# Kernel tuning notes

Measured on AMD Instinct MI355X. Metric: run time of the kernel, lower is better.

The kernel has to match this reference:

```python
import jax, jax.numpy as jnp
import numpy as np

T = 8192        # tokens (batch*seq)
D = 1024        # d_model
H = 4096        # expert hidden = 4*d_model
E = 16          # num_expert
K = 2           # moe_top_k


def setup_inputs() -> dict:
    key = jax.random.key(0)
    ks = jax.random.split(key, 7)
    s_in = 1.0 / np.sqrt(D)
    s_h = 1.0 / np.sqrt(H)
    return {
        "moe_inp": jax.random.normal(ks[0], (T, D), dtype=jnp.float32),
        "Wg": jax.random.normal(ks[1], (D, E), dtype=jnp.float32) * s_in,
        "bg": jnp.zeros((E,), dtype=jnp.float32),
        "W1": jax.random.normal(ks[2], (E, D, H), dtype=jnp.float32) * s_in,
        "b1": jnp.zeros((E, H), dtype=jnp.float32),
        "W2": jax.random.normal(ks[3], (E, H, D), dtype=jnp.float32) * s_h,
        "b2": jnp.zeros((E, D), dtype=jnp.float32),
    }


def reference(moe_inp, Wg, bg, W1, b1, W2, b2):
    # --- NaiveGate: linear -> top-k -> softmax over selected logits ---
    logits = moe_inp @ Wg + bg                      # [T, E]
    topk_val, topk_idx = jax.lax.top_k(logits, K)   # [T, K]
    gate_score = jax.nn.softmax(topk_val, axis=-1)  # [T, K]

    # Per-(token, expert) combine weight: sum of gate scores of slots routed to e.
    # Equivalent to scatter(dispatch) -> expert MLP -> gather(combine) weighted sum.
    onehot = jax.nn.one_hot(topk_idx, E, dtype=moe_inp.dtype)  # [T, K, E]
    comb_w = jnp.einsum('tk,tke->te', gate_score, onehot)      # [T, E]

    out = jnp.zeros_like(moe_inp)
    for e in range(E):  # fixed small expert count
        h = jax.nn.relu(moe_inp @ W1[e] + b1[e])   # [T, H]
        y = h @ W2[e] + b2[e]                      # [T, D]
        out = out + comb_w[:, e:e + 1] * y
    return out
```

## Files before the change

kernel.cpp:

```cpp
#include <hip/hip_runtime.h>
#include <hip/hip_bf16.h>
#include <stdint.h>


#define Tn 8192
#define Dn 1024
#define Hn 4096
#define En 16

typedef __attribute__((ext_vector_type(8))) short bf16x8;
typedef __attribute__((ext_vector_type(4))) float f32x4;

__device__ __forceinline__ unsigned short f2bf(float f) {
    union { __hip_bfloat16 h; unsigned short u; } cv;
    cv.h = __float2bfloat16(f);
    return cv.u;
}

__device__ __forceinline__ void gload_lds16(const void* gptr, void* lptr) {
    __builtin_amdgcn_global_load_lds(
        (const __attribute__((address_space(1))) uint32_t*)gptr,
        (__attribute__((address_space(3))) uint32_t*)lptr, 16, 0, 0);
}

__device__ __forceinline__ int find_e(const int* __restrict__ mb, int gm) {
    int e = 0;
#pragma unroll
    for (int i = 1; i < En; i++) e += (mb[i] <= gm) ? 1 : 0;
    return e;
}

__device__ __forceinline__ void waitvm8() { asm volatile("s_waitcnt vmcnt(8)" ::: "memory"); }
__device__ __forceinline__ void waitvm4() { asm volatile("s_waitcnt vmcnt(4)" ::: "memory"); }
__device__ __forceinline__ void waitvm0() { asm volatile("s_waitcnt vmcnt(0)" ::: "memory"); }
__device__ __forceinline__ void waitlgkm0() { asm volatile("s_waitcnt lgkmcnt(0)" ::: "memory"); }
__device__ __forceinline__ void barrier_raw() { asm volatile("s_barrier" ::: "memory"); }

__device__ __forceinline__ bool better(float va, int ia, float vb, int ib) {
    return (va > vb) || (va == vb && ia < ib);
}

__global__ __launch_bounds__(256) void gate_kernel(
    const float* __restrict__ x, const float* __restrict__ Wg,
    const float* __restrict__ bg,
    int* cnt, int* tok_e, int* tok_pos, float* tok_w)
{
    __shared__ float wgt[16 * 1028];
    int tid = threadIdx.x;
    int t0 = blockIdx.x * 16;

#pragma unroll
    for (int i = 0; i < 64; i++) {
        int idx = i * 256 + tid;
        int k = idx >> 4, e = idx & 15;
        wgt[e * 1028 + k] = Wg[idx];
    }
    __syncthreads();

    int tok = tid >> 4, e = tid & 15;
    const float4* xr = reinterpret_cast<const float4*>(x + (size_t)(t0 + tok) * Dn);
    const float4* wr = reinterpret_cast<const float4*>(&wgt[e * 1028]);
    float acc = 0.f;
#pragma unroll 8
    for (int q = 0; q < 256; q++) {
        float4 xv = xr[q], wv = wr[q];
        acc += xv.x * wv.x + xv.y * wv.y + xv.z * wv.z + xv.w * wv.w;
    }
    acc += bg[e];

    float v0 = acc, v1 = -1e30f;
    int i0 = e, i1 = -1;
#pragma unroll
    for (int m = 1; m < 16; m <<= 1) {
        float ov0 = __shfl_xor(v0, m, 16); int oi0 = __shfl_xor(i0, m, 16);
        float ov1 = __shfl_xor(v1, m, 16); int oi1 = __shfl_xor(i1, m, 16);
        if (better(ov0, oi0, v0, i0)) {
            if (better(v0, i0, ov1, oi1)) { v1 = v0; i1 = i0; }
            else                          { v1 = ov1; i1 = oi1; }
            v0 = ov0; i0 = oi0;
        } else if (better(ov0, oi0, v1, i1)) {
            v1 = ov0; i1 = oi0;
        }
    }
    if (e == 0) {
        float ex = __expf(v1 - v0);
        float w0 = 1.f / (1.f + ex);
        float w1 = ex / (1.f + ex);
        int p0 = atomicAdd(&cnt[i0], 1);
        int p1 = atomicAdd(&cnt[i1], 1);
        int t = t0 + tok;
        tok_e[t * 2 + 0] = i0; tok_e[t * 2 + 1] = i1;
        tok_pos[t * 2 + 0] = p0; tok_pos[t * 2 + 1] = p1;
        tok_w[t * 2 + 0] = w0; tok_w[t * 2 + 1] = w1;
    }
}

__global__ void scan_kernel(const int* cnt, int* base, int* mb)
{
    if (threadIdx.x == 0 && blockIdx.x == 0) {
        int b = 0, m = 0;
        for (int e = 0; e < En; e++) {
            base[e] = b; mb[e] = m;
            b += cnt[e];
            m += (cnt[e] + 255) >> 8;
        }
        base[En] = b; mb[En] = m;
    }
}

__global__ __launch_bounds__(256) void gather_kernel(
    const float* __restrict__ x, const int* tok_e, const int* tok_pos,
    const int* base, unsigned short* xg)
{
    int t = blockIdx.x; int tid = threadIdx.x;
    int e0 = tok_e[2 * t], e1 = tok_e[2 * t + 1];
    int r0 = base[e0] + tok_pos[2 * t];
    int r1 = base[e1] + tok_pos[2 * t + 1];
    float4 v = *reinterpret_cast<const float4*>(x + (size_t)t * Dn + tid * 4);
    ushort4 u;
    u.x = f2bf(v.x); u.y = f2bf(v.y); u.z = f2bf(v.z); u.w = f2bf(v.w);
    *reinterpret_cast<ushort4*>(xg + (size_t)r0 * Dn + tid * 4) = u;
    *reinterpret_cast<ushort4*>(xg + (size_t)r1 * Dn + tid * 4) = u;
}

__global__ __launch_bounds__(512) void convT_kernel(
    const float* __restrict__ src, unsigned short* __restrict__ dst, int R, int C)
{
    int e = blockIdx.z;
    const float* s = src + (size_t)e * R * C;
    unsigned short* d = dst + (size_t)e * R * C;
    __shared__ float tile[64][65];
    int r0 = blockIdx.y * 64, c0 = blockIdx.x * 64;
    int tr = threadIdx.x >> 4;
    int tc4 = (threadIdx.x & 15) * 4;
    float4 v0 = *reinterpret_cast<const float4*>(s + (size_t)(r0 + tr) * C + c0 + tc4);
    float4 v1 = *reinterpret_cast<const float4*>(s + (size_t)(r0 + tr + 32) * C + c0 + tc4);
    tile[tr][tc4 + 0] = v0.x; tile[tr][tc4 + 1] = v0.y;
    tile[tr][tc4 + 2] = v0.z; tile[tr][tc4 + 3] = v0.w;
    tile[tr + 32][tc4 + 0] = v1.x; tile[tr + 32][tc4 + 1] = v1.y;
    tile[tr + 32][tc4 + 2] = v1.z; tile[tr + 32][tc4 + 3] = v1.w;
    __syncthreads();
    ushort4 u0, u1;
    u0.x = f2bf(tile[tc4 + 0][tr]);      u1.x = f2bf(tile[tc4 + 0][tr + 32]);
    u0.y = f2bf(tile[tc4 + 1][tr]);      u1.y = f2bf(tile[tc4 + 1][tr + 32]);
    u0.z = f2bf(tile[tc4 + 2][tr]);      u1.z = f2bf(tile[tc4 + 2][tr + 32]);
    u0.w = f2bf(tile[tc4 + 3][tr]);      u1.w = f2bf(tile[tc4 + 3][tr + 32]);
    *reinterpret_cast<ushort4*>(d + (size_t)(c0 + tr) * R + r0 + tc4) = u0;
    *reinterpret_cast<ushort4*>(d + (size_t)(c0 + tr + 32) * R + r0 + tc4) = u1;
}

template<bool G1>
__global__ __launch_bounds__(512, 2) void gemm8p_kernel(
    const unsigned short* __restrict__ Ag, const unsigned short* __restrict__ Bg,
    const float* __restrict__ bias, unsigned short* __restrict__ outb,
    float* __restrict__ outf, size_t ystride,
    const int* __restrict__ cnt, const int* __restrict__ base,
    const int* __restrict__ mb)
{
    constexpr int KDIM = G1 ? Dn : Hn;
    constexpr int KLEN = G1 ? Dn : (Hn / 2);
    constexpr int NOUT = G1 ? Hn : Dn;
    constexpr int NT = KLEN / 32;
    __shared__ unsigned short ldsA[4][256 * 32];
    __shared__ unsigned short ldsB[4][256 * 32];

    int bid = blockIdx.x;
    int xcd = bid & 7;
    int slot = bid >> 3;
    int totalgm = mb[En];
    int rounds = G1 ? ((totalgm + 15) >> 4) : ((totalgm + 31) >> 5);

    int tid = threadIdx.x;
    int lane = tid & 63;
    int wid = tid >> 6;
    int wr = wid >> 2, wc = wid & 3;
    int lr16 = lane & 15, lk = lane >> 4;
    int lj = (lane >> 4) * 4;

    int ja0 = tid;        int ra0 = ja0 >> 2; int ca0 = (ja0 & 3) ^ ((ra0 >> 1) & 3);
    int ja1 = tid + 512;  int ra1 = ja1 >> 2; int ca1 = (ja1 & 3) ^ ((ra1 >> 1) & 3);

    int aoff[8], boff[4];
#pragma unroll
    for (int m = 0; m < 8; m++) {
        int row = wr * 128 + m * 16 + lr16;
        aoff[m] = row * 32 + ((lk ^ ((row >> 1) & 3)) << 3);
    }
#pragma unroll
    for (int n = 0; n < 4; n++) {
        int row = wc * 64 + n * 16 + lr16;
        boff[n] = row * 32 + ((lk ^ ((row >> 1) & 3)) << 3);
    }

    for (int r = 0; r < rounds; r++) {
        int gm, ntile, kh;
        if constexpr (G1) {
            gm = r * 16 + (slot >> 1);
            ntile = xcd * 2 + (slot & 1);
            kh = 0;
        } else {
            gm = r * 32 + slot;
            ntile = xcd >> 1;
            kh = xcd & 1;
        }
        if (gm >= totalgm) continue;

        int e = find_e(mb, gm);
        int mtile = gm - mb[e];
        int M_e = cnt[e];
        int m0 = mtile * 256, n0 = ntile * 256;
        int kbase = kh * KLEN;
        int rowbase0 = base[e] + m0;
        const unsigned short* Ab = Ag + (size_t)rowbase0 * KDIM + kbase;
        const unsigned short* Bb = Bg + (size_t)e * NOUT * KDIM + (size_t)n0 * KDIM + kbase;

        const unsigned short* aSrc0 = Ab + (size_t)ra0 * KDIM + ca0 * 8;
        const unsigned short* aSrc1 = Ab + (size_t)ra1 * KDIM + ca1 * 8;
        const unsigned short* bSrc0 = Bb + (size_t)ra0 * KDIM + ca0 * 8;
        const unsigned short* bSrc1 = Bb + (size_t)ra1 * KDIM + ca1 * 8;

        f32x4 acc[8][4];
#pragma unroll
        for (int m = 0; m < 8; m++)
#pragma unroll
            for (int n = 0; n < 4; n++) acc[m][n] = (f32x4){0.f, 0.f, 0.f, 0.f};

        auto stageA = [&](int t) {
            char* sa = (char*)ldsA[t & 3];
            int k0 = t * 32;
            gload_lds16(aSrc0 + k0, sa + ja0 * 16);
            gload_lds16(aSrc1 + k0, sa + ja1 * 16);
        };
        auto stageB = [&](int t) {
            char* sb = (char*)ldsB[t & 3];
            int k0 = t * 32;
            gload_lds16(bSrc0 + k0, sb + ja0 * 16);
            gload_lds16(bSrc1 + k0, sb + ja1 * 16);
        };

        stageB(0); stageA(0);
        stageB(1); stageA(1);
        stageB(2); stageA(2);
        waitvm8();
        barrier_raw();

#pragma unroll 4
        for (int t = 0; t < NT; ++t) {
            const unsigned short* sa = ldsA[t & 3];
            const unsigned short* sb = ldsB[t & 3];
            bf16x8 a[4], b[4];
#pragma unroll
            for (int m = 0; m < 4; m++) a[m] = *(const bf16x8*)(sa + aoff[m]);
#pragma unroll
            for (int n = 0; n < 4; n++) b[n] = *(const bf16x8*)(sb + boff[n]);
            if (t + 3 < NT) stageB(t + 3);
            barrier_raw();
            waitlgkm0();
            __builtin_amdgcn_s_setprio(1);
#pragma unroll
            for (int m = 0; m < 4; m++)
#pragma unroll
                for (int n = 0; n < 4; n++)
                    acc[m][n] = __builtin_amdgcn_mfma_f32_16x16x32_bf16(b[n], a[m], acc[m][n], 0, 0, 0);
            __builtin_amdgcn_s_setprio(0);
            barrier_raw();
#pragma unroll
            for (int m = 0; m < 4; m++) a[m] = *(const bf16x8*)(sa + aoff[m + 4]);
            if (t + 3 < NT) stageA(t + 3);
            barrier_raw();
            waitlgkm0();
            __builtin_amdgcn_s_setprio(1);
#pragma unroll
            for (int m = 0; m < 4; m++)
#pragma unroll
                for (int n = 0; n < 4; n++)
                    acc[m + 4][n] = __builtin_amdgcn_mfma_f32_16x16x32_bf16(b[n], a[m], acc[m + 4][n], 0, 0, 0);
            __builtin_amdgcn_s_setprio(0);
            if (t < NT - 3)       waitvm8();
            else if (t == NT - 3) waitvm4();
            else if (t == NT - 2) waitvm0();
            barrier_raw();
        }

        bool addb = G1 || (kh == 0);
        const float* be = bias + (size_t)e * NOUT;
        float* yb = outf + (G1 ? 0 : (size_t)kh * ystride);
#pragma unroll
        for (int m = 0; m < 8; m++) {
            int rt = wr * 128 + m * 16 + lr16;
            if (m0 + rt < M_e) {
                size_t rowoff = (size_t)(rowbase0 + rt) * NOUT;
#pragma unroll
                for (int n = 0; n < 4; n++) {
                    int col0 = n0 + wc * 64 + n * 16 + lj;
                    float4 bs = addb ? *reinterpret_cast<const float4*>(be + col0)
                                     : (float4){0.f, 0.f, 0.f, 0.f};
                    float v0 = acc[m][n][0] + bs.x;
                    float v1 = acc[m][n][1] + bs.y;
                    float v2 = acc[m][n][2] + bs.z;
                    float v3 = acc[m][n][3] + bs.w;
                    if constexpr (G1) {
                        ushort4 u;
                        u.x = f2bf(fmaxf(v0, 0.f));
                        u.y = f2bf(fmaxf(v1, 0.f));
                        u.z = f2bf(fmaxf(v2, 0.f));
                        u.w = f2bf(fmaxf(v3, 0.f));
                        *reinterpret_cast<ushort4*>(outb + rowoff + col0) = u;
                    } else {
                        float4 o = {v0, v1, v2, v3};
                        *reinterpret_cast<float4*>(yb + rowoff + col0) = o;
                    }
                }
            }
        }
    }
}

__global__ __launch_bounds__(256) void combine_kernel(
    const float* __restrict__ y, size_t ystride,
    const int* __restrict__ tok_e, const int* __restrict__ tok_pos,
    const int* __restrict__ base, const float* __restrict__ tok_w,
    float* __restrict__ out)
{
    int t = blockIdx.x, tid = threadIdx.x;
    int e0 = tok_e[2 * t], e1 = tok_e[2 * t + 1];
    int r0 = base[e0] + tok_pos[2 * t];
    int r1 = base[e1] + tok_pos[2 * t + 1];
    float w0 = tok_w[2 * t], w1 = tok_w[2 * t + 1];
    const float* y1 = y + ystride;
    float4 a0 = *reinterpret_cast<const float4*>(y  + (size_t)r0 * Dn + tid * 4);
    float4 a1 = *reinterpret_cast<const float4*>(y1 + (size_t)r0 * Dn + tid * 4);
    float4 b0 = *reinterpret_cast<const float4*>(y  + (size_t)r1 * Dn + tid * 4);
    float4 b1 = *reinterpret_cast<const float4*>(y1 + (size_t)r1 * Dn + tid * 4);
    float4 o;
    o.x = w0 * (a0.x + a1.x) + w1 * (b0.x + b1.x);
    o.y = w0 * (a0.y + a1.y) + w1 * (b0.y + b1.y);
    o.z = w0 * (a0.z + a1.z) + w1 * (b0.z + b1.z);
    o.w = w0 * (a0.w + a1.w) + w1 * (b0.w + b1.w);
    *reinterpret_cast<float4*>(out + (size_t)t * Dn + tid * 4) = o;
}

extern "C" void kernel_launch(void* const* d_in, const int* in_sizes, int n_in,
                              void* d_out, int out_size, void* d_ws, size_t ws_size,
                              hipStream_t stream)
{
    const float* x  = (const float*)d_in[0];
    const float* Wg = (const float*)d_in[1];
    const float* bg = (const float*)d_in[2];
    const float* W1 = (const float*)d_in[3];
    const float* b1 = (const float*)d_in[4];
    const float* W2 = (const float*)d_in[5];
    const float* b2 = (const float*)d_in[6];
    float* out = (float*)d_out;

    char* ws = (char*)d_ws;
    size_t off = 0;
    auto alloc = [&](size_t bytes) {
        size_t o = off; off += (bytes + 255) & ~(size_t)255; return o;
    };
    const int ROWS = Tn * 2;
    const int RCAP = ROWS + 256;
    const size_t YSTR = (size_t)RCAP * Dn;

    unsigned short* Wt = (unsigned short*)(ws + alloc((size_t)En * Hn * Dn * 2));
    unsigned short* xg = (unsigned short*)(ws + alloc((size_t)RCAP * Dn * 2));
    unsigned short* hg = (unsigned short*)(ws + alloc((size_t)RCAP * Hn * 2));
    float* yv      = (float*)(ws + alloc(2 * YSTR * 4));
    int*   cnt     = (int*)(ws + alloc(En * 4));
    int*   base    = (int*)(ws + alloc((En + 1) * 4));
    int*   mb      = (int*)(ws + alloc((En + 1) * 4));
    int*   tok_e   = (int*)(ws + alloc(Tn * 2 * 4));
    int*   tok_pos = (int*)(ws + alloc(Tn * 2 * 4));
    float* tok_w   = (float*)(ws + alloc(Tn * 2 * 4));
    (void)ws_size; (void)in_sizes; (void)n_in; (void)out_size;

    hipMemsetAsync(cnt, 0, En * 4, stream);

    gate_kernel<<<Tn / 16, 256, 0, stream>>>(x, Wg, bg, cnt, tok_e, tok_pos, tok_w);
    scan_kernel<<<1, 64, 0, stream>>>(cnt, base, mb);
    gather_kernel<<<Tn, 256, 0, stream>>>(x, tok_e, tok_pos, base, xg);

    convT_kernel<<<dim3(Hn / 64, Dn / 64, En), 512, 0, stream>>>(W1, Wt, Dn, Hn);
    gemm8p_kernel<true><<<256, 512, 0, stream>>>(
        xg, Wt, b1, hg, nullptr, 0, cnt, base, mb);

    convT_kernel<<<dim3(Dn / 64, Hn / 64, En), 512, 0, stream>>>(W2, Wt, Hn, Dn);
    gemm8p_kernel<false><<<256, 512, 0, stream>>>(
        hg, Wt, b2, nullptr, yv, YSTR, cnt, base, mb);

    combine_kernel<<<Tn, 256, 0, stream>>>(yv, YSTR, tok_e, tok_pos, base, tok_w, out);
}
```

Baseline: 737.2 us.

## Switch grouped GEMM to BK=64 double-buffered pipeline and bf16 partial outputs

Restructures the expert GEMM main loop from a 4-stage BK=32 pipeline with split A/B staging and several barriers per step into a 2-stage BK=64 double buffer. It uses one vmcnt(0) wait and one barrier per K step, with an 8-way XOR swizzle on LDS rows. The second GEMM now writes its split-K partial results as bf16 instead of fp32, and the combine kernel reads them back as bf16. This halves the partial-output write and read traffic, at the cost of extra rounding in the partial sums. The shallower pipeline also risks exposing more global-load latency.

After: 753.1 us. 2.2% more time.

```diff
diff --git a/kernel.cpp b/kernel.cpp
--- a/kernel.cpp
+++ b/kernel.cpp
@@ -16,6 +16,11 @@
     cv.h = __float2bfloat16(f);
     return cv.u;
 }
+__device__ __forceinline__ float bf2f(unsigned short u) {
+    union { unsigned int i; float f; } cv;
+    cv.i = ((unsigned int)u) << 16;
+    return cv.f;
+}
 
 __device__ __forceinline__ void gload_lds16(const void* gptr, void* lptr) {
     __builtin_amdgcn_global_load_lds(
@@ -30,10 +35,7 @@
     return e;
 }
 
-__device__ __forceinline__ void waitvm8() { asm volatile("s_waitcnt vmcnt(8)" ::: "memory"); }
-__device__ __forceinline__ void waitvm4() { asm volatile("s_waitcnt vmcnt(4)" ::: "memory"); }
-__device__ __forceinline__ void waitvm0() { asm volatile("s_waitcnt vmcnt(0)" ::: "memory"); }
-__device__ __forceinline__ void waitlgkm0() { asm volatile("s_waitcnt lgkmcnt(0)" ::: "memory"); }
+__device__ __forceinline__ void waitvm0()  { asm volatile("s_waitcnt vmcnt(0)" ::: "memory"); }
 __device__ __forceinline__ void barrier_raw() { asm volatile("s_barrier" ::: "memory"); }
 
 __device__ __forceinline__ bool better(float va, int ia, float vb, int ib) {
@@ -150,19 +152,19 @@
 }
 
 template<bool G1>
-__global__ __launch_bounds__(512, 2) void gemm8p_kernel(
+__global__ __launch_bounds__(512, 2) void gemmk_kernel(
     const unsigned short* __restrict__ Ag, const unsigned short* __restrict__ Bg,
     const float* __restrict__ bias, unsigned short* __restrict__ outb,
-    float* __restrict__ outf, size_t ystride,
+    size_t ystride,
     const int* __restrict__ cnt, const int* __restrict__ base,
     const int* __restrict__ mb)
 {
     constexpr int KDIM = G1 ? Dn : Hn;
     constexpr int KLEN = G1 ? Dn : (Hn / 2);
     constexpr int NOUT = G1 ? Hn : Dn;
-    constexpr int NT = KLEN / 32;
-    __shared__ unsigned short ldsA[4][256 * 32];
-    __shared__ unsigned short ldsB[4][256 * 32];
+    constexpr int NT = KLEN / 64;
+    __shared__ unsigned short ldsA[2][256 * 64];
+    __shared__ unsigned short ldsB[2][256 * 64];
 
     int bid = blockIdx.x;
     int xcd = bid & 7;
@@ -175,21 +177,25 @@
     int wid = tid >> 6;
     int wr = wid >> 2, wc = wid & 3;
     int lr16 = lane & 15, lk = lane >> 4;
-    int lj = (lane >> 4) * 4;
-
-    int ja0 = tid;        int ra0 = ja0 >> 2; int ca0 = (ja0 & 3) ^ ((ra0 >> 1) & 3);
-    int ja1 = tid + 512;  int ra1 = ja1 >> 2; int ca1 = (ja1 & 3) ^ ((ra1 >> 1) & 3);
-
-    int aoff[8], boff[4];
+    int lj = lk * 4;
+
+    int r0t = tid >> 3;
+    int col8 = (tid & 7) ^ (r0t & 7);
+
+    int aoff[8][2], boff[4][2];
 #pragma unroll
     for (int m = 0; m < 8; m++) {
         int row = wr * 128 + m * 16 + lr16;
-        aoff[m] = row * 32 + ((lk ^ ((row >> 1) & 3)) << 3);
+#pragma unroll
+        for (int kk = 0; kk < 2; kk++)
+            aoff[m][kk] = row * 64 + (((kk * 4 + lk) ^ (row & 7)) << 3);
     }
 #pragma unroll
     for (int n = 0; n < 4; n++) {
         int row = wc * 64 + n * 16 + lr16;
-        boff[n] = row * 32 + ((lk ^ ((row >> 1) & 3)) << 3);
+#pragma unroll
+        for (int kk = 0; kk < 2; kk++)
+            boff[n][kk] = row * 64 + (((kk * 4 + lk) ^ (row & 7)) << 3);
     }
 
     for (int r = 0; r < rounds; r++) {
@@ -214,10 +220,8 @@
         const unsigned short* Ab = Ag + (size_t)rowbase0 * KDIM + kbase;
         const unsigned short* Bb = Bg + (size_t)e * NOUT * KDIM + (size_t)n0 * KDIM + kbase;
 
-        const unsigned short* aSrc0 = Ab + (size_t)ra0 * KDIM + ca0 * 8;
-        const unsigned short* aSrc1 = Ab + (size_t)ra1 * KDIM + ca1 * 8;
-        const unsigned short* bSrc0 = Bb + (size_t)ra0 * KDIM + ca0 * 8;
-        const unsigned short* bSrc1 = Bb + (size_t)ra1 * KDIM + ca1 * 8;
+        const unsigned short* aSrc = Ab + (size_t)r0t * KDIM + col8 * 8;
+        const unsigned short* bSrc = Bb + (size_t)r0t * KDIM + col8 * 8;
 
         f32x4 acc[8][4];
 #pragma unroll
@@ -225,66 +229,55 @@
 #pragma unroll
             for (int n = 0; n < 4; n++) acc[m][n] = (f32x4){0.f, 0.f, 0.f, 0.f};
 
-        auto stageA = [&](int t) {
-            char* sa = (char*)ldsA[t & 3];
-            int k0 = t * 32;
-            gload_lds16(aSrc0 + k0, sa + ja0 * 16);
-            gload_lds16(aSrc1 + k0, sa + ja1 * 16);
+        auto stage = [&](int t) {
+            char* sa = (char*)ldsA[t & 1];
+            char* sb = (char*)ldsB[t & 1];
+            int k0 = t * 64;
+#pragma unroll
+            for (int i = 0; i < 4; i++) {
+                gload_lds16(aSrc + (size_t)(i * 64) * KDIM + k0, sa + (tid + i * 512) * 16);
+                gload_lds16(bSrc + (size_t)(i * 64) * KDIM + k0, sb + (tid + i * 512) * 16);
+            }
         };
-        auto stageB = [&](int t) {
-            char* sb = (char*)ldsB[t & 3];
-            int k0 = t * 32;
-            gload_lds16(bSrc0 + k0, sb + ja0 * 16);
-            gload_lds16(bSrc1 + k0, sb + ja1 * 16);
-        };
-
-        stageB(0); stageA(0);
-        stageB(1); stageA(1);
-        stageB(2); stageA(2);
-        waitvm8();
-        barrier_raw();
-
-#pragma unroll 4
+
+        stage(0);
+
         for (int t = 0; t < NT; ++t) {
-            const unsigned short* sa = ldsA[t & 3];
-            const unsigned short* sb = ldsB[t & 3];
-            bf16x8 a[4], b[4];
-#pragma unroll
-            for (int m = 0; m < 4; m++) a[m] = *(const bf16x8*)(sa + aoff[m]);
-#pragma unroll
-            for (int n = 0; n < 4; n++) b[n] = *(const bf16x8*)(sb + boff[n]);
-            if (t + 3 < NT) stageB(t + 3);
+            waitvm0();
             barrier_raw();
-            waitlgkm0();
-            __builtin_amdgcn_s_setprio(1);
-#pragma unroll
-            for (int m = 0; m < 4; m++)
-#pragma unroll
-                for (int n = 0; n < 4; n++)
-                    acc[m][n] = __builtin_amdgcn_mfma_f32_16x16x32_bf16(b[n], a[m], acc[m][n], 0, 0, 0);
-            __builtin_amdgcn_s_setprio(0);
-            barrier_raw();
-#pragma unroll
-            for (int m = 0; m < 4; m++) a[m] = *(const bf16x8*)(sa + aoff[m + 4]);
-            if (t + 3 < NT) stageA(t + 3);
-            barrier_raw();
-            waitlgkm0();
-            __builtin_amdgcn_s_setprio(1);
-#pragma unroll
-            for (int m = 0; m < 4; m++)
-#pragma unroll
-                for (int n = 0; n < 4; n++)
-                    acc[m + 4][n] = __builtin_amdgcn_mfma_f32_16x16x32_bf16(b[n], a[m], acc[m + 4][n], 0, 0, 0);
-            __builtin_amdgcn_s_setprio(0);
-            if (t < NT - 3)       waitvm8();
-            else if (t == NT - 3) waitvm4();
-            else if (t == NT - 2) waitvm0();
-            barrier_raw();
+            if (t + 1 < NT) stage(t + 1);
+            asm volatile("" ::: "memory");
+            const unsigned short* sa = ldsA[t & 1];
+            const unsigned short* sb = ldsB[t & 1];
+#pragma unroll
+            for (int kk = 0; kk < 2; kk++) {
+                bf16x8 a[4], b[4];
+#pragma unroll
+                for (int n = 0; n < 4; n++) b[n] = *(const bf16x8*)(sb + boff[n][kk]);
+#pragma unroll
+                for (int m = 0; m < 4; m++) a[m] = *(const bf16x8*)(sa + aoff[m][kk]);
+                __builtin_amdgcn_s_setprio(1);
+#pragma unroll
+                for (int m = 0; m < 4; m++)
+#pragma unroll
+                    for (int n = 0; n < 4; n++)
+                        acc[m][n] = __builtin_amdgcn_mfma_f32_16x16x32_bf16(b[n], a[m], acc[m][n], 0, 0, 0);
+                __builtin_amdgcn_s_setprio(0);
+#pragma unroll
+                for (int m = 0; m < 4; m++) a[m] = *(const bf16x8*)(sa + aoff[m + 4][kk]);
+                __builtin_amdgcn_s_setprio(1);
+#pragma unroll
+                for (int m = 0; m < 4; m++)
+#pragma unroll
+                    for (int n = 0; n < 4; n++)
+                        acc[m + 4][n] = __builtin_amdgcn_mfma_f32_16x16x32_bf16(b[n], a[m], acc[m + 4][n], 0, 0, 0);
+                __builtin_amdgcn_s_setprio(0);
+            }
         }
 
         bool addb = G1 || (kh == 0);
         const float* be = bias + (size_t)e * NOUT;
-        float* yb = outf + (G1 ? 0 : (size_t)kh * ystride);
+        unsigned short* ob = outb + (G1 ? 0 : (size_t)kh * ystride);
 #pragma unroll
         for (int m = 0; m < 8; m++) {
             int rt = wr * 128 + m * 16 + lr16;
@@ -299,17 +292,17 @@
                     float v1 = acc[m][n][1] + bs.y;
                     float v2 = acc[m][n][2] + bs.z;
                     float v3 = acc[m][n][3] + bs.w;
+                    ushort4 u;
                     if constexpr (G1) {
-                        ushort4 u;
                         u.x = f2bf(fmaxf(v0, 0.f));
                         u.y = f2bf(fmaxf(v1, 0.f));
                         u.z = f2bf(fmaxf(v2, 0.f));
                         u.w = f2bf(fmaxf(v3, 0.f));
-                        *reinterpret_cast<ushort4*>(outb + rowoff + col0) = u;
                     } else {
-                        float4 o = {v0, v1, v2, v3};
-                        *reinterpret_cast<float4*>(yb + rowoff + col0) = o;
+                        u.x = f2bf(v0); u.y = f2bf(v1);
+                        u.z = f2bf(v2); u.w = f2bf(v3);
                     }
+                    *reinterpret_cast<ushort4*>(ob + rowoff + col0) = u;
                 }
             }
         }
@@ -317,7 +310,7 @@
 }
 
 __global__ __launch_bounds__(256) void combine_kernel(
-    const float* __restrict__ y, size_t ystride,
+    const unsigned short* __restrict__ y, size_t ystride,
     const int* __restrict__ tok_e, const int* __restrict__ tok_pos,
     const int* __restrict__ base, const float* __restrict__ tok_w,
     float* __restrict__ out)
@@ -327,16 +320,16 @@
     int r0 = base[e0] + tok_pos[2 * t];
     int r1 = base[e1] + tok_pos[2 * t + 1];
     float w0 = tok_w[2 * t], w1 = tok_w[2 * t + 1];
-    const float* y1 = y + ystride;
-    float4 a0 = *reinterpret_cast<const float4*>(y  + (size_t)r0 * Dn + tid * 4);
-    float4 a1 = *reinterpret_cast<const float4*>(y1 + (size_t)r0 * Dn + tid * 4);
-    float4 b0 = *reinterpret_cast<const float4*>(y  + (size_t)r1 * Dn + tid * 4);
-    float4 b1 = *reinterpret_cast<const float4*>(y1 + (size_t)r1 * Dn + tid * 4);
+    const unsigned short* y1 = y + ystride;
+    ushort4 a0 = *reinterpret_cast<const ushort4*>(y  + (size_t)r0 * Dn + tid * 4);
+    ushort4 a1 = *reinterpret_cast<const ushort4*>(y1 + (size_t)r0 * Dn + tid * 4);
+    ushort4 b0 = *reinterpret_cast<const ushort4*>(y  + (size_t)r1 * Dn + tid * 4);
+    ushort4 b1 = *reinterpret_cast<const ushort4*>(y1 + (size_t)r1 * Dn + tid * 4);
     float4 o;
-    o.x = w0 * (a0.x + a1.x) + w1 * (b0.x + b1.x);
-    o.y = w0 * (a0.y + a1.y) + w1 * (b0.y + b1.y);
-    o.z = w0 * (a0.z + a1.z) + w1 * (b0.z + b1.z);
-    o.w = w0 * (a0.w + a1.w) + w1 * (b0.w + b1.w);
+    o.x = w0 * (bf2f(a0.x) + bf2f(a1.x)) + w1 * (bf2f(b0.x) + bf2f(b1.x));
+    o.y = w0 * (bf2f(a0.y) + bf2f(a1.y)) + w1 * (bf2f(b0.y) + bf2f(b1.y));
+    o.z = w0 * (bf2f(a0.z) + bf2f(a1.z)) + w1 * (bf2f(b0.z) + bf2f(b1.z));
+    o.w = w0 * (bf2f(a0.w) + bf2f(a1.w)) + w1 * (bf2f(b0.w) + bf2f(b1.w));
     *reinterpret_cast<float4*>(out + (size_t)t * Dn + tid * 4) = o;
 }
 
@@ -365,7 +358,7 @@
     unsigned short* Wt = (unsigned short*)(ws + alloc((size_t)En * Hn * Dn * 2));
     unsigned short* xg = (unsigned short*)(ws + alloc((size_t)RCAP * Dn * 2));
     unsigned short* hg = (unsigned short*)(ws + alloc((size_t)RCAP * Hn * 2));
-    float* yv      = (float*)(ws + alloc(2 * YSTR * 4));
+    unsigned short* yv = (unsigned short*)(ws + alloc(2 * YSTR * 2));
     int*   cnt     = (int*)(ws + alloc(En * 4));
     int*   base    = (int*)(ws + alloc((En + 1) * 4));
     int*   mb      = (int*)(ws + alloc((En + 1) * 4));
@@ -381,12 +374,12 @@
     gather_kernel<<<Tn, 256, 0, stream>>>(x, tok_e, tok_pos, base, xg);
 
     convT_kernel<<<dim3(Hn / 64, Dn / 64, En), 512, 0, stream>>>(W1, Wt, Dn, Hn);
-    gemm8p_kernel<true><<<256, 512, 0, stream>>>(
-        xg, Wt, b1, hg, nullptr, 0, cnt, base, mb);
+    gemmk_kernel<true><<<256, 512, 0, stream>>>(
+        xg, Wt, b1, hg, 0, cnt, base, mb);
 
     convT_kernel<<<dim3(Dn / 64, Hn / 64, En), 512, 0, stream>>>(W2, Wt, Hn, Dn);
-    gemm8p_kernel<false><<<256, 512, 0, stream>>>(
-        hg, Wt, b2, nullptr, yv, YSTR, cnt, base, mb);
+    gemmk_kernel<false><<<256, 512, 0, stream>>>(
+        hg, Wt, b2, yv, YSTR, cnt, base, mb);
 
     combine_kernel<<<Tn, 256, 0, stream>>>(yv, YSTR, tok_e, tok_pos, base, tok_w, out);
 }
```
